# Optimization experiments

Hardware: AMD Instinct MI355X
Metric: run time of the kernel (lower is better)

## Reference

```python
import jax, jax.numpy as jnp
import numpy as np

TEMPERATURE = 0.07
LOSS_CL_WEIGHT = 1.0
EPS = 1e-12  # F.normalize default eps


def setup_inputs() -> dict:
    key = jax.random.key(0)
    k1, k2 = jax.random.split(key)
    N, S, D = 64, 64, 256
    return {
        "proj_z1": jax.random.normal(k1, (N, S, D), dtype=jnp.float32),
        "proj_z2": jax.random.normal(k2, (N, S, D), dtype=jnp.float32),
    }


def _clean_normalize(x, NS, D):
    # flatten -> replace nan/inf with 0 -> L2 normalize rows
    x = x.reshape(NS, D)
    x = jnp.where(jnp.isfinite(x), x, jnp.zeros((), x.dtype))
    norm = jnp.linalg.norm(x, axis=1, keepdims=True)
    return x / jnp.maximum(norm, EPS)


def reference(proj_z1, proj_z2):
    N, S, D = proj_z1.shape
    NS = N * S
    M = 2 * NS
    f1 = _clean_normalize(proj_z1, NS, D)
    f2 = _clean_normalize(proj_z2, NS, D)
    features = jnp.concatenate([f1, f2], axis=0)          # (M, D)
    sim = features @ features.T                            # (M, M)

    idx = jnp.arange(M)
    # positive pair: row i <-> row (i + NS) mod M (eye blocks in label_matrix)
    positives = sim[idx, (idx + NS) % M] / TEMPERATURE     # (M,)
    # CE denominator = all off-diagonal entries (positives + negatives)
    scores = sim / TEMPERATURE
    scores = jnp.where(idx[:, None] == idx[None, :], -jnp.inf, scores)
    lse = jax.nn.logsumexp(scores, axis=1)                 # (M,)
    loss = jnp.mean(lse - positives)
    return LOSS_CL_WEIGHT * loss
```

## Files before the change

kernel.cpp:

```cpp
#include <hip/hip_runtime.h>
#include <hip/hip_bf16.h>
#include <stdint.h>

#define NS_ 4096
#define M_  8192
#define D_  256
#define TEMP 0.07f
#define EXP_SCALE 20.61707212818536f
#define LN2 0.6931471805599453f

typedef short bf16x8 __attribute__((ext_vector_type(8)));
typedef float f32x4  __attribute__((ext_vector_type(4)));
typedef unsigned short ushortx4 __attribute__((ext_vector_type(4)));

static __device__ inline unsigned short f2bf(float x) {
    unsigned u = __float_as_uint(x);
    u += 0x7fffu + ((u >> 16) & 1u);
    return (unsigned short)(u >> 16);
}

static __device__ inline float cleanf(float v) {
    return __builtin_isfinite(v) ? v : 0.0f;
}

#define LDS_LOAD16(gp, lp) \
    __builtin_amdgcn_global_load_lds((const __attribute__((address_space(1))) uint32_t*)(gp), \
                                     (__attribute__((address_space(3))) uint32_t*)(lp), 16, 0, 0)

__global__ __launch_bounds__(64) void knorm(const float* __restrict__ z1,
                                            const float* __restrict__ z2,
                                            short* __restrict__ F,
                                            float* __restrict__ pos,
                                            float* __restrict__ denom,
                                            int* __restrict__ cnt,
                                            float* __restrict__ out) {
    const int i = blockIdx.x;
    const int t = threadIdx.x;
    const float4* p1 = (const float4*)(z1 + (size_t)i * D_);
    const float4* p2 = (const float4*)(z2 + (size_t)i * D_);
    float4 a = p1[t], b = p2[t];
    a.x = cleanf(a.x); a.y = cleanf(a.y); a.z = cleanf(a.z); a.w = cleanf(a.w);
    b.x = cleanf(b.x); b.y = cleanf(b.y); b.z = cleanf(b.z); b.w = cleanf(b.w);

    float s1 = a.x*a.x + a.y*a.y + a.z*a.z + a.w*a.w;
    float s2 = b.x*b.x + b.y*b.y + b.z*b.z + b.w*b.w;
    float dp = a.x*b.x + a.y*b.y + a.z*b.z + a.w*b.w;
    #pragma unroll
    for (int m = 1; m < 64; m <<= 1) {
        s1 += __shfl_xor(s1, m);
        s2 += __shfl_xor(s2, m);
        dp += __shfl_xor(dp, m);
    }
    const float inv1 = 1.0f / fmaxf(sqrtf(s1), 1e-12f);
    const float inv2 = 1.0f / fmaxf(sqrtf(s2), 1e-12f);

    ushortx4 o1, o2;
    o1.x = f2bf(a.x * inv1); o1.y = f2bf(a.y * inv1); o1.z = f2bf(a.z * inv1); o1.w = f2bf(a.w * inv1);
    o2.x = f2bf(b.x * inv2); o2.y = f2bf(b.y * inv2); o2.z = f2bf(b.z * inv2); o2.w = f2bf(b.w * inv2);
    ((ushortx4*)(F + (size_t)i * D_))[t]          = o1;
    ((ushortx4*)(F + (size_t)(i + NS_) * D_))[t]  = o2;

    if (t == 0) pos[i] = dp * inv1 * inv2;
    if (t < 2)  denom[i * 2 + t] = 0.0f;
    if (i == 0 && t < 32) cnt[t] = 0;
    if (i == 0 && t == 0) out[0] = 0.0f;
}

__global__ __launch_bounds__(256, 2) void kgemm(const short* __restrict__ F,
                                                float* __restrict__ denom,
                                                int* __restrict__ cnt,
                                                const float* __restrict__ pos,
                                                float* __restrict__ out) {
    __shared__ short Bl[64 * 256];
    __shared__ int lastflag;
    __shared__ float red[4];

    const int rtile = blockIdx.x >> 4;
    const int cq    = blockIdx.x & 15;
    const int R0 = rtile * 256;
    const int C0 = cq * 512;

    const int tid  = threadIdx.x;
    const int lane = tid & 63;
    const int wave = tid >> 6;
    const int c16  = lane & 15;
    const int quad = lane >> 4;
    const int swz  = c16 & 7;

    int goff[8];
    #pragma unroll
    for (int r2 = 0; r2 < 8; ++r2) {
        int c    = tid + r2 * 256;
        int row  = c >> 5;
        int kg   = (c & 31) ^ (row & 7);
        goff[r2] = row * D_ + kg * 8;
    }

    bf16x8 afrag[4][8];
    const int arow_l = wave * 16 + c16;
    #pragma unroll
    for (int ch = 0; ch < 4; ++ch) {
        __syncthreads();
        const short* ga = F + (size_t)(R0 + ch * 64) * D_;
        #pragma unroll
        for (int r2 = 0; r2 < 8; ++r2)
            LDS_LOAD16(ga + goff[r2], Bl + (tid + r2 * 256) * 8);
        __syncthreads();
        #pragma unroll
        for (int ks = 0; ks < 8; ++ks)
            afrag[ch][ks] = *(const bf16x8*)(Bl + arow_l * 256 +
                                             (((ks * 4 + quad) ^ (arow_l & 7)) * 8));
    }

    float accexp[4][4];
    #pragma unroll
    for (int s = 0; s < 4; ++s)
        #pragma unroll
        for (int r = 0; r < 4; ++r) accexp[s][r] = 0.0f;

    for (int it = 0; it < 8; ++it) {
        __syncthreads();
        const short* gb = F + (size_t)(C0 + it * 64) * D_;
        #pragma unroll
        for (int r2 = 0; r2 < 8; ++r2)
            LDS_LOAD16(gb + goff[r2], Bl + (tid + r2 * 256) * 8);
        __syncthreads();

        #pragma unroll
        for (int sub = 0; sub < 4; ++sub) {
            const int tc = sub * 16 + c16;
            bf16x8 bfrag[8];
            #pragma unroll
            for (int ks = 0; ks < 8; ++ks)
                bfrag[ks] = *(const bf16x8*)(Bl + tc * 256 +
                                             (((ks * 4 + quad) ^ swz) * 8));
            f32x4 acc[4];
            #pragma unroll
            for (int s = 0; s < 4; ++s) acc[s] = (f32x4){0.f, 0.f, 0.f, 0.f};
            #pragma unroll
            for (int ks = 0; ks < 8; ++ks)
                #pragma unroll
                for (int s = 0; s < 4; ++s)
                    acc[s] = __builtin_amdgcn_mfma_f32_16x16x32_bf16(
                        afrag[s][ks], bfrag[ks], acc[s], 0, 0, 0);

            const int colbase = C0 + it * 64 + sub * 16;
            #pragma unroll
            for (int s = 0; s < 4; ++s) {
                const int rowbase = R0 + s * 64 + wave * 16;
                if (colbase != rowbase) {
                    #pragma unroll
                    for (int r = 0; r < 4; ++r)
                        accexp[s][r] += __builtin_amdgcn_exp2f(acc[s][r] * EXP_SCALE);
                } else {
                    #pragma unroll
                    for (int r = 0; r < 4; ++r) {
                        float e = __builtin_amdgcn_exp2f(acc[s][r] * EXP_SCALE);
                        if (c16 == quad * 4 + r) e = 0.0f;
                        accexp[s][r] += e;
                    }
                }
            }
        }
    }

    #pragma unroll
    for (int s = 0; s < 4; ++s)
        #pragma unroll
        for (int r = 0; r < 4; ++r) {
            float v = accexp[s][r];
            v += __shfl_xor(v, 1);
            v += __shfl_xor(v, 2);
            v += __shfl_xor(v, 4);
            v += __shfl_xor(v, 8);
            if (c16 == 0)
                atomicAdd(&denom[R0 + s * 64 + wave * 16 + quad * 4 + r], v);
        }

    __syncthreads();
    if (tid == 0) {
        __threadfence();
        lastflag = (atomicAdd(&cnt[rtile], 1) == 15);
    }
    __syncthreads();
    if (lastflag) {
        __threadfence();
        float v = atomicAdd(&denom[R0 + tid], 0.0f);
        float p = __builtin_amdgcn_logf(v) * (LN2 / (float)M_);
        #pragma unroll
        for (int m = 1; m < 64; m <<= 1) p += __shfl_xor(p, m);
        if (lane == 0) red[wave] = p;
        __syncthreads();
        if (tid == 0) atomicAdd(out, red[0] + red[1] + red[2] + red[3]);
        if (rtile == 0) {
            __syncthreads();
            float sp = 0.0f;
            for (int i = tid; i < NS_; i += 256) sp += pos[i];
            #pragma unroll
            for (int m = 1; m < 64; m <<= 1) sp += __shfl_xor(sp, m);
            if (lane == 0) red[wave] = sp;
            __syncthreads();
            if (tid == 0)
                atomicAdd(out, (red[0] + red[1] + red[2] + red[3]) *
                               (-2.0f / (TEMP * (float)M_)));
        }
    }
}

extern "C" void kernel_launch(void* const* d_in, const int* in_sizes, int n_in,
                              void* d_out, int out_size, void* d_ws, size_t ws_size,
                              hipStream_t stream) {
    const float* z1 = (const float*)d_in[0];
    const float* z2 = (const float*)d_in[1];

    short* F     = (short*)d_ws;
    float* denom = (float*)((char*)d_ws + (size_t)M_ * D_ * 2);
    int*   cnt   = (int*)(denom + M_);
    float* pos   = (float*)(cnt + 32);
    float* out   = (float*)d_out;

    knorm<<<NS_, 64, 0, stream>>>(z1, z2, F, pos, denom, cnt, out);
    kgemm<<<512, 256, 0, stream>>>(F, denom, cnt, pos, out);
}
```

Baseline: 108.4 us.

## Double-buffer LDS tile loads in GEMM and batch four rows per norm block

The GEMM kernel now double-buffers the shared-memory tile. It issues the global-to-LDS load for the next 64-row tile before waiting on the current one, using explicit vmcnt waits and raw barriers, so load latency overlaps MFMA and exp work. MFMA sections also raise wave priority with s_setprio. The normalization kernel processes four rows per 256-thread block instead of one row per 64-thread block, which cuts the block count. Doubling LDS to 64 KB per block could limit occupancy, and the hand-written waitcnt counts are fragile if the compiler reorders memory ops.

```diff
diff --git a/kernel.cpp b/kernel.cpp
--- a/kernel.cpp
+++ b/kernel.cpp
@@ -1,5 +1,4 @@
 #include <hip/hip_runtime.h>
-#include <hip/hip_bf16.h>
 #include <stdint.h>
 
 #define NS_ 4096
@@ -27,15 +26,16 @@
     __builtin_amdgcn_global_load_lds((const __attribute__((address_space(1))) uint32_t*)(gp), \
                                      (__attribute__((address_space(3))) uint32_t*)(lp), 16, 0, 0)
 
-__global__ __launch_bounds__(64) void knorm(const float* __restrict__ z1,
-                                            const float* __restrict__ z2,
-                                            short* __restrict__ F,
-                                            float* __restrict__ pos,
-                                            float* __restrict__ denom,
-                                            int* __restrict__ cnt,
-                                            float* __restrict__ out) {
-    const int i = blockIdx.x;
-    const int t = threadIdx.x;
+__global__ __launch_bounds__(256) void knorm(const float* __restrict__ z1,
+                                             const float* __restrict__ z2,
+                                             short* __restrict__ F,
+                                             float* __restrict__ pos,
+                                             float* __restrict__ denom,
+                                             int* __restrict__ cnt,
+                                             float* __restrict__ out) {
+    const int wave = threadIdx.x >> 6;
+    const int t    = threadIdx.x & 63;
+    const int i    = blockIdx.x * 4 + wave;
     const float4* p1 = (const float4*)(z1 + (size_t)i * D_);
     const float4* p2 = (const float4*)(z2 + (size_t)i * D_);
     float4 a = p1[t], b = p2[t];
@@ -71,7 +71,7 @@
                                                 int* __restrict__ cnt,
                                                 const float* __restrict__ pos,
                                                 float* __restrict__ out) {
-    __shared__ short Bl[64 * 256];
+    __shared__ short Bl[2][64 * 256];
     __shared__ int lastflag;
     __shared__ float red[4];
 
@@ -96,20 +96,33 @@
         goff[r2] = row * D_ + kg * 8;
     }
 
+    const short* baseA = F + (size_t)R0 * D_;
+    const short* baseB = F + (size_t)C0 * D_;
+
+    auto STAGE = [&](const short* g, int buf) {
+        short* l = &Bl[buf][0];
+        #pragma unroll
+        for (int r2 = 0; r2 < 8; ++r2)
+            LDS_LOAD16(g + goff[r2], l + (tid + r2 * 256) * 8);
+    };
+
+    STAGE(baseA, 0);
+
     bf16x8 afrag[4][8];
     const int arow_l = wave * 16 + c16;
     #pragma unroll
     for (int ch = 0; ch < 4; ++ch) {
-        __syncthreads();
-        const short* ga = F + (size_t)(R0 + ch * 64) * D_;
-        #pragma unroll
-        for (int r2 = 0; r2 < 8; ++r2)
-            LDS_LOAD16(ga + goff[r2], Bl + (tid + r2 * 256) * 8);
-        __syncthreads();
+        const short* nxt = (ch < 3) ? (baseA + (size_t)(ch + 1) * 64 * D_) : baseB;
+        STAGE(nxt, (ch + 1) & 1);
+        asm volatile("s_waitcnt vmcnt(8)" ::: "memory");
+        __builtin_amdgcn_s_barrier();
+        const short* bp = &Bl[ch & 1][0];
         #pragma unroll
         for (int ks = 0; ks < 8; ++ks)
-            afrag[ch][ks] = *(const bf16x8*)(Bl + arow_l * 256 +
+            afrag[ch][ks] = *(const bf16x8*)(bp + arow_l * 256 +
                                              (((ks * 4 + quad) ^ (arow_l & 7)) * 8));
+        asm volatile("s_waitcnt lgkmcnt(0)" ::: "memory");
+        __builtin_amdgcn_s_barrier();
     }
 
     float accexp[4][4];
@@ -119,12 +132,14 @@
         for (int r = 0; r < 4; ++r) accexp[s][r] = 0.0f;
 
     for (int it = 0; it < 8; ++it) {
-        __syncthreads();
-        const short* gb = F + (size_t)(C0 + it * 64) * D_;
-        #pragma unroll
-        for (int r2 = 0; r2 < 8; ++r2)
-            LDS_LOAD16(gb + goff[r2], Bl + (tid + r2 * 256) * 8);
-        __syncthreads();
+        if (it < 7) {
+            STAGE(baseB + (size_t)(it + 1) * 64 * D_, (it + 1) & 1);
+            asm volatile("s_waitcnt vmcnt(8)" ::: "memory");
+        } else {
+            asm volatile("s_waitcnt vmcnt(0)" ::: "memory");
+        }
+        __builtin_amdgcn_s_barrier();
+        const short* bp = &Bl[it & 1][0];
 
         #pragma unroll
         for (int sub = 0; sub < 4; ++sub) {
@@ -132,17 +147,19 @@
             bf16x8 bfrag[8];
             #pragma unroll
             for (int ks = 0; ks < 8; ++ks)
-                bfrag[ks] = *(const bf16x8*)(Bl + tc * 256 +
+                bfrag[ks] = *(const bf16x8*)(bp + tc * 256 +
                                              (((ks * 4 + quad) ^ swz) * 8));
             f32x4 acc[4];
             #pragma unroll
             for (int s = 0; s < 4; ++s) acc[s] = (f32x4){0.f, 0.f, 0.f, 0.f};
+            __builtin_amdgcn_s_setprio(1);
             #pragma unroll
             for (int ks = 0; ks < 8; ++ks)
                 #pragma unroll
                 for (int s = 0; s < 4; ++s)
                     acc[s] = __builtin_amdgcn_mfma_f32_16x16x32_bf16(
                         afrag[s][ks], bfrag[ks], acc[s], 0, 0, 0);
+            __builtin_amdgcn_s_setprio(0);
 
             const int colbase = C0 + it * 64 + sub * 16;
             #pragma unroll
@@ -162,6 +179,8 @@
                 }
             }
         }
+        asm volatile("s_waitcnt lgkmcnt(0)" ::: "memory");
+        __builtin_amdgcn_s_barrier();
     }
 
     #pragma unroll
@@ -219,6 +238,6 @@
     float* pos   = (float*)(cnt + 32);
     float* out   = (float*)d_out;
 
-    knorm<<<NS_, 64, 0, stream>>>(z1, z2, F, pos, denom, cnt, out);
+    knorm<<<NS_ / 4, 256, 0, stream>>>(z1, z2, F, pos, denom, cnt, out);
     kgemm<<<512, 256, 0, stream>>>(F, denom, cnt, pos, out);
 }
```

Result: slower. 114.6 us (+5.7%).

## Fuse normalize and GEMM-LSE into one cooperative kernel with grid syncs

Applied to the files above, without the earlier changes.

Merges the normalization kernel and the similarity/logsumexp kernel into a single cooperative launch of 512 blocks. Grid-wide syncs separate the phases and replace the per-row-tile counter used for the final reduction. This removes one kernel launch and the gap between the two kernels. In exchange it adds two grid barriers and needs all blocks to be co-resident; if the cooperative launch fails, the old two-kernel path runs instead.

```diff
diff --git a/kernel.cpp b/kernel.cpp
--- a/kernel.cpp
+++ b/kernel.cpp
@@ -1,6 +1,8 @@
 #include <hip/hip_runtime.h>
-#include <hip/hip_bf16.h>
+#include <hip/hip_cooperative_groups.h>
 #include <stdint.h>
+
+namespace cg = cooperative_groups;
 
 #define NS_ 4096
 #define M_  8192
@@ -27,62 +29,66 @@
     __builtin_amdgcn_global_load_lds((const __attribute__((address_space(1))) uint32_t*)(gp), \
                                      (__attribute__((address_space(3))) uint32_t*)(lp), 16, 0, 0)
 
-__global__ __launch_bounds__(64) void knorm(const float* __restrict__ z1,
-                                            const float* __restrict__ z2,
-                                            short* __restrict__ F,
-                                            float* __restrict__ pos,
-                                            float* __restrict__ denom,
-                                            int* __restrict__ cnt,
-                                            float* __restrict__ out) {
-    const int i = blockIdx.x;
-    const int t = threadIdx.x;
-    const float4* p1 = (const float4*)(z1 + (size_t)i * D_);
-    const float4* p2 = (const float4*)(z2 + (size_t)i * D_);
-    float4 a = p1[t], b = p2[t];
-    a.x = cleanf(a.x); a.y = cleanf(a.y); a.z = cleanf(a.z); a.w = cleanf(a.w);
-    b.x = cleanf(b.x); b.y = cleanf(b.y); b.z = cleanf(b.z); b.w = cleanf(b.w);
-
-    float s1 = a.x*a.x + a.y*a.y + a.z*a.z + a.w*a.w;
-    float s2 = b.x*b.x + b.y*b.y + b.z*b.z + b.w*b.w;
-    float dp = a.x*b.x + a.y*b.y + a.z*b.z + a.w*b.w;
-    #pragma unroll
-    for (int m = 1; m < 64; m <<= 1) {
-        s1 += __shfl_xor(s1, m);
-        s2 += __shfl_xor(s2, m);
-        dp += __shfl_xor(dp, m);
-    }
-    const float inv1 = 1.0f / fmaxf(sqrtf(s1), 1e-12f);
-    const float inv2 = 1.0f / fmaxf(sqrtf(s2), 1e-12f);
-
-    ushortx4 o1, o2;
-    o1.x = f2bf(a.x * inv1); o1.y = f2bf(a.y * inv1); o1.z = f2bf(a.z * inv1); o1.w = f2bf(a.w * inv1);
-    o2.x = f2bf(b.x * inv2); o2.y = f2bf(b.y * inv2); o2.z = f2bf(b.z * inv2); o2.w = f2bf(b.w * inv2);
-    ((ushortx4*)(F + (size_t)i * D_))[t]          = o1;
-    ((ushortx4*)(F + (size_t)(i + NS_) * D_))[t]  = o2;
-
-    if (t == 0) pos[i] = dp * inv1 * inv2;
-    if (t < 2)  denom[i * 2 + t] = 0.0f;
-    if (i == 0 && t < 32) cnt[t] = 0;
-    if (i == 0 && t == 0) out[0] = 0.0f;
-}
-
-__global__ __launch_bounds__(256, 2) void kgemm(const short* __restrict__ F,
-                                                float* __restrict__ denom,
-                                                int* __restrict__ cnt,
-                                                const float* __restrict__ pos,
-                                                float* __restrict__ out) {
+#define STORE_AGENT_U64(p, v) \
+    __hip_atomic_store((uint64_t*)(p), (v), __ATOMIC_RELAXED, __HIP_MEMORY_SCOPE_AGENT)
+#define STORE_AGENT_F32(p, v) \
+    __hip_atomic_store((float*)(p), (v), __ATOMIC_RELAXED, __HIP_MEMORY_SCOPE_AGENT)
+
+__global__ __launch_bounds__(256, 2) void kfused(const float* __restrict__ z1,
+                                                 const float* __restrict__ z2,
+                                                 short* __restrict__ F,
+                                                 float* __restrict__ pos,
+                                                 float* __restrict__ denom,
+                                                 float* __restrict__ out) {
     __shared__ short Bl[64 * 256];
-    __shared__ int lastflag;
     __shared__ float red[4];
-
-    const int rtile = blockIdx.x >> 4;
-    const int cq    = blockIdx.x & 15;
-    const int R0 = rtile * 256;
-    const int C0 = cq * 512;
 
     const int tid  = threadIdx.x;
     const int lane = tid & 63;
     const int wave = tid >> 6;
+    const int bid  = blockIdx.x;
+
+    #pragma unroll
+    for (int pp = 0; pp < 2; ++pp) {
+        const int i = bid * 8 + wave * 2 + pp;
+        float4 a = ((const float4*)(z1 + (size_t)i * D_))[lane];
+        float4 b = ((const float4*)(z2 + (size_t)i * D_))[lane];
+        a.x = cleanf(a.x); a.y = cleanf(a.y); a.z = cleanf(a.z); a.w = cleanf(a.w);
+        b.x = cleanf(b.x); b.y = cleanf(b.y); b.z = cleanf(b.z); b.w = cleanf(b.w);
+
+        float s1 = a.x*a.x + a.y*a.y + a.z*a.z + a.w*a.w;
+        float s2 = b.x*b.x + b.y*b.y + b.z*b.z + b.w*b.w;
+        float dp = a.x*b.x + a.y*b.y + a.z*b.z + a.w*b.w;
+        #pragma unroll
+        for (int m = 1; m < 64; m <<= 1) {
+            s1 += __shfl_xor(s1, m);
+            s2 += __shfl_xor(s2, m);
+            dp += __shfl_xor(dp, m);
+        }
+        const float inv1 = 1.0f / fmaxf(sqrtf(s1), 1e-12f);
+        const float inv2 = 1.0f / fmaxf(sqrtf(s2), 1e-12f);
+
+        uint64_t u1 = (uint64_t)f2bf(a.x * inv1)
+                    | ((uint64_t)f2bf(a.y * inv1) << 16)
+                    | ((uint64_t)f2bf(a.z * inv1) << 32)
+                    | ((uint64_t)f2bf(a.w * inv1) << 48);
+        uint64_t u2 = (uint64_t)f2bf(b.x * inv2)
+                    | ((uint64_t)f2bf(b.y * inv2) << 16)
+                    | ((uint64_t)f2bf(b.z * inv2) << 32)
+                    | ((uint64_t)f2bf(b.w * inv2) << 48);
+        STORE_AGENT_U64((uint64_t*)(F + (size_t)i * D_) + lane, u1);
+        STORE_AGENT_U64((uint64_t*)(F + (size_t)(i + NS_) * D_) + lane, u2);
+        if (lane == 0) STORE_AGENT_F32(pos + i, dp * inv1 * inv2);
+    }
+    if (tid < 16) STORE_AGENT_F32(denom + bid * 16 + tid, 0.0f);
+    if (bid == 0 && tid == 0) STORE_AGENT_F32(out, 0.0f);
+    __threadfence();
+    cg::this_grid().sync();
+
+    const int rtile = bid >> 4;
+    const int cq    = bid & 15;
+    const int R0 = rtile * 256;
+    const int C0 = cq * 512;
     const int c16  = lane & 15;
     const int quad = lane >> 4;
     const int swz  = c16 & 7;
@@ -177,25 +183,22 @@
                 atomicAdd(&denom[R0 + s * 64 + wave * 16 + quad * 4 + r], v);
         }
 
-    __syncthreads();
-    if (tid == 0) {
-        __threadfence();
-        lastflag = (atomicAdd(&cnt[rtile], 1) == 15);
-    }
-    __syncthreads();
-    if (lastflag) {
-        __threadfence();
-        float v = atomicAdd(&denom[R0 + tid], 0.0f);
+    __threadfence();
+    cg::this_grid().sync();
+
+    if (bid < 32) {
+        float v = atomicAdd(&denom[bid * 256 + tid], 0.0f);
         float p = __builtin_amdgcn_logf(v) * (LN2 / (float)M_);
         #pragma unroll
         for (int m = 1; m < 64; m <<= 1) p += __shfl_xor(p, m);
         if (lane == 0) red[wave] = p;
         __syncthreads();
         if (tid == 0) atomicAdd(out, red[0] + red[1] + red[2] + red[3]);
-        if (rtile == 0) {
+        if (bid == 0) {
             __syncthreads();
             float sp = 0.0f;
-            for (int i = tid; i < NS_; i += 256) sp += pos[i];
+            for (int ii = tid; ii < NS_; ii += 256)
+                sp += atomicAdd(&pos[ii], 0.0f);
             #pragma unroll
             for (int m = 1; m < 64; m <<= 1) sp += __shfl_xor(sp, m);
             if (lane == 0) red[wave] = sp;
@@ -207,6 +210,186 @@
     }
 }
 
+__global__ __launch_bounds__(64) void knorm(const float* __restrict__ z1,
+                                            const float* __restrict__ z2,
+                                            short* __restrict__ F,
+                                            float* __restrict__ pos,
+                                            float* __restrict__ denom,
+                                            int* __restrict__ cnt,
+                                            float* __restrict__ out) {
+    const int i = blockIdx.x;
+    const int t = threadIdx.x;
+    const float4* p1 = (const float4*)(z1 + (size_t)i * D_);
+    const float4* p2 = (const float4*)(z2 + (size_t)i * D_);
+    float4 a = p1[t], b = p2[t];
+    a.x = cleanf(a.x); a.y = cleanf(a.y); a.z = cleanf(a.z); a.w = cleanf(a.w);
+    b.x = cleanf(b.x); b.y = cleanf(b.y); b.z = cleanf(b.z); b.w = cleanf(b.w);
+
+    float s1 = a.x*a.x + a.y*a.y + a.z*a.z + a.w*a.w;
+    float s2 = b.x*b.x + b.y*b.y + b.z*b.z + b.w*b.w;
+    float dp = a.x*b.x + a.y*b.y + a.z*b.z + a.w*b.w;
+    #pragma unroll
+    for (int m = 1; m < 64; m <<= 1) {
+        s1 += __shfl_xor(s1, m);
+        s2 += __shfl_xor(s2, m);
+        dp += __shfl_xor(dp, m);
+    }
+    const float inv1 = 1.0f / fmaxf(sqrtf(s1), 1e-12f);
+    const float inv2 = 1.0f / fmaxf(sqrtf(s2), 1e-12f);
+
+    ushortx4 o1, o2;
+    o1.x = f2bf(a.x * inv1); o1.y = f2bf(a.y * inv1); o1.z = f2bf(a.z * inv1); o1.w = f2bf(a.w * inv1);
+    o2.x = f2bf(b.x * inv2); o2.y = f2bf(b.y * inv2); o2.z = f2bf(b.z * inv2); o2.w = f2bf(b.w * inv2);
+    ((ushortx4*)(F + (size_t)i * D_))[t]          = o1;
+    ((ushortx4*)(F + (size_t)(i + NS_) * D_))[t]  = o2;
+
+    if (t == 0) pos[i] = dp * inv1 * inv2;
+    if (t < 2)  denom[i * 2 + t] = 0.0f;
+    if (i == 0 && t < 32) cnt[t] = 0;
+    if (i == 0 && t == 0) out[0] = 0.0f;
+}
+
+__global__ __launch_bounds__(256, 2) void kgemm(const short* __restrict__ F,
+                                                float* __restrict__ denom,
+                                                int* __restrict__ cnt,
+                                                const float* __restrict__ pos,
+                                                float* __restrict__ out) {
+    __shared__ short Bl[64 * 256];
+    __shared__ int lastflag;
+    __shared__ float red[4];
+
+    const int rtile = blockIdx.x >> 4;
+    const int cq    = blockIdx.x & 15;
+    const int R0 = rtile * 256;
+    const int C0 = cq * 512;
+
+    const int tid  = threadIdx.x;
+    const int lane = tid & 63;
+    const int wave = tid >> 6;
+    const int c16  = lane & 15;
+    const int quad = lane >> 4;
+    const int swz  = c16 & 7;
+
+    int goff[8];
+    #pragma unroll
+    for (int r2 = 0; r2 < 8; ++r2) {
+        int c    = tid + r2 * 256;
+        int row  = c >> 5;
+        int kg   = (c & 31) ^ (row & 7);
+        goff[r2] = row * D_ + kg * 8;
+    }
+
+    bf16x8 afrag[4][8];
+    const int arow_l = wave * 16 + c16;
+    #pragma unroll
+    for (int ch = 0; ch < 4; ++ch) {
+        __syncthreads();
+        const short* ga = F + (size_t)(R0 + ch * 64) * D_;
+        #pragma unroll
+        for (int r2 = 0; r2 < 8; ++r2)
+            LDS_LOAD16(ga + goff[r2], Bl + (tid + r2 * 256) * 8);
+        __syncthreads();
+        #pragma unroll
+        for (int ks = 0; ks < 8; ++ks)
+            afrag[ch][ks] = *(const bf16x8*)(Bl + arow_l * 256 +
+                                             (((ks * 4 + quad) ^ (arow_l & 7)) * 8));
+    }
+
+    float accexp[4][4];
+    #pragma unroll
+    for (int s = 0; s < 4; ++s)
+        #pragma unroll
+        for (int r = 0; r < 4; ++r) accexp[s][r] = 0.0f;
+
+    for (int it = 0; it < 8; ++it) {
+        __syncthreads();
+        const short* gb = F + (size_t)(C0 + it * 64) * D_;
+        #pragma unroll
+        for (int r2 = 0; r2 < 8; ++r2)
+            LDS_LOAD16(gb + goff[r2], Bl + (tid + r2 * 256) * 8);
+        __syncthreads();
+
+        #pragma unroll
+        for (int sub = 0; sub < 4; ++sub) {
+            const int tc = sub * 16 + c16;
+            bf16x8 bfrag[8];
+            #pragma unroll
+            for (int ks = 0; ks < 8; ++ks)
+                bfrag[ks] = *(const bf16x8*)(Bl + tc * 256 +
+                                             (((ks * 4 + quad) ^ swz) * 8));
+            f32x4 acc[4];
+            #pragma unroll
+            for (int s = 0; s < 4; ++s) acc[s] = (f32x4){0.f, 0.f, 0.f, 0.f};
+            #pragma unroll
+            for (int ks = 0; ks < 8; ++ks)
+                #pragma unroll
+                for (int s = 0; s < 4; ++s)
+                    acc[s] = __builtin_amdgcn_mfma_f32_16x16x32_bf16(
+                        afrag[s][ks], bfrag[ks], acc[s], 0, 0, 0);
+
+            const int colbase = C0 + it * 64 + sub * 16;
+            #pragma unroll
+            for (int s = 0; s < 4; ++s) {
+                const int rowbase = R0 + s * 64 + wave * 16;
+                if (colbase != rowbase) {
+                    #pragma unroll
+                    for (int r = 0; r < 4; ++r)
+                        accexp[s][r] += __builtin_amdgcn_exp2f(acc[s][r] * EXP_SCALE);
+                } else {
+                    #pragma unroll
+                    for (int r = 0; r < 4; ++r) {
+                        float e = __builtin_amdgcn_exp2f(acc[s][r] * EXP_SCALE);
+                        if (c16 == quad * 4 + r) e = 0.0f;
+                        accexp[s][r] += e;
+                    }
+                }
+            }
+        }
+    }
+
+    #pragma unroll
+    for (int s = 0; s < 4; ++s)
+        #pragma unroll
+        for (int r = 0; r < 4; ++r) {
+            float v = accexp[s][r];
+            v += __shfl_xor(v, 1);
+            v += __shfl_xor(v, 2);
+            v += __shfl_xor(v, 4);
+            v += __shfl_xor(v, 8);
+            if (c16 == 0)
+                atomicAdd(&denom[R0 + s * 64 + wave * 16 + quad * 4 + r], v);
+        }
+
+    __syncthreads();
+    if (tid == 0) {
+        __threadfence();
+        lastflag = (atomicAdd(&cnt[rtile], 1) == 15);
+    }
+    __syncthreads();
+    if (lastflag) {
+        __threadfence();
+        float v = atomicAdd(&denom[R0 + tid], 0.0f);
+        float p = __builtin_amdgcn_logf(v) * (LN2 / (float)M_);
+        #pragma unroll
+        for (int m = 1; m < 64; m <<= 1) p += __shfl_xor(p, m);
+        if (lane == 0) red[wave] = p;
+        __syncthreads();
+        if (tid == 0) atomicAdd(out, red[0] + red[1] + red[2] + red[3]);
+        if (rtile == 0) {
+            __syncthreads();
+            float sp = 0.0f;
+            for (int i = tid; i < NS_; i += 256) sp += pos[i];
+            #pragma unroll
+            for (int m = 1; m < 64; m <<= 1) sp += __shfl_xor(sp, m);
+            if (lane == 0) red[wave] = sp;
+            __syncthreads();
+            if (tid == 0)
+                atomicAdd(out, (red[0] + red[1] + red[2] + red[3]) *
+                               (-2.0f / (TEMP * (float)M_)));
+        }
+    }
+}
+
 extern "C" void kernel_launch(void* const* d_in, const int* in_sizes, int n_in,
                               void* d_out, int out_size, void* d_ws, size_t ws_size,
                               hipStream_t stream) {
@@ -217,8 +400,14 @@
     float* denom = (float*)((char*)d_ws + (size_t)M_ * D_ * 2);
     int*   cnt   = (int*)(denom + M_);
     float* pos   = (float*)(cnt + 32);
-    float* out   = (float*)d_out;
-
-    knorm<<<NS_, 64, 0, stream>>>(z1, z2, F, pos, denom, cnt, out);
-    kgemm<<<512, 256, 0, stream>>>(F, denom, cnt, pos, out);
-}
+    float* outp  = (float*)d_out;
+
+    void* args[] = { (void*)&z1, (void*)&z2, (void*)&F, (void*)&pos,
+                     (void*)&denom, (void*)&outp };
+    hipError_t e = hipLaunchCooperativeKernel((const void*)kfused, dim3(512), dim3(256),
+                                              args, 0, stream);
+    if (e != hipSuccess) {
+        knorm<<<NS_, 64, 0, stream>>>(z1, z2, F, pos, denom, cnt, outp);
+        kgemm<<<512, 256, 0, stream>>>(F, denom, cnt, pos, outp);
+    }
+}
```

After: 301.1 us. 2.78x slower.
